# Kernel optimization log

Hardware: AMD Instinct MI355X
Metric: run time of the kernel (lower is better)

## Reference

```python
import jax, jax.numpy as jnp
import numpy as np

D_MODEL = 1024   # 'seq_len' arg = input feature dim
FF_DIM = 1024
SCALE = 0.03125  # 1/sqrt(1024)


def setup_inputs() -> dict:
    key = jax.random.key(0)
    ks = jax.random.split(key, 7)
    B, T = 8, 2048
    s = 1.0 / np.sqrt(D_MODEL)
    return {
        "sequence": jax.random.normal(ks[0], (B, T, D_MODEL), dtype=jnp.float32),
        "Wq": jax.random.uniform(ks[1], (FF_DIM, D_MODEL), jnp.float32, -s, s),
        "bq": jax.random.uniform(ks[2], (FF_DIM,), jnp.float32, -s, s),
        "Wk": jax.random.uniform(ks[3], (FF_DIM, D_MODEL), jnp.float32, -s, s),
        "bk": jax.random.uniform(ks[4], (FF_DIM,), jnp.float32, -s, s),
        "Wv": jax.random.uniform(ks[5], (FF_DIM, D_MODEL), jnp.float32, -s, s),
        "bv": jax.random.uniform(ks[6], (FF_DIM,), jnp.float32, -s, s),
    }


def reference(sequence, Wq, bq, Wk, bk, Wv, bv):
    # Q/K/V linear projections (torch Linear: x @ W.T + b)
    q = jnp.einsum('btd,fd->btf', sequence, Wq) + bq
    k = jnp.einsum('btd,fd->btf', sequence, Wk) + bk
    v = jnp.einsum('btd,fd->btf', sequence, Wv) + bv
    # scaled dot-product attention (dropout p=0 -> identity)
    scores = jnp.einsum('btf,bsf->bts', q, k) * SCALE  # [B,T,T]
    attn = jax.nn.softmax(scores, axis=-1)
    return jnp.einsum('bts,bsf->btf', attn, v)
```

## Files before the change

kernel.cpp:

```cpp
#include <hip/hip_runtime.h>
#include <hip/hip_bf16.h>

#define BB 8
#define TT 2048
#define DD 1024
#define FF 1024

typedef __attribute__((ext_vector_type(8))) short bf16x8;
typedef __attribute__((ext_vector_type(4))) float f32x4;
typedef __attribute__((ext_vector_type(4))) short s16x4;

constexpr float kScaleLog2e = 0.03125f * 1.44269504088896340736f;

__device__ __forceinline__ short bf16_bits(float x) {
    __hip_bfloat16 h = __float2bfloat16(x);
    short s;
    __builtin_memcpy(&s, &h, sizeof(short));
    return s;
}

__global__ __launch_bounds__(256) void cvt_kernel(
    const float* __restrict__ src, short* __restrict__ dst, int n8)
{
    const int i = blockIdx.x * 256 + threadIdx.x;
    if (i < n8) {
        f32x4 a = ((const f32x4*)src)[2 * i];
        f32x4 b = ((const f32x4*)src)[2 * i + 1];
        bf16x8 o;
#pragma unroll
        for (int j = 0; j < 4; ++j) { o[j] = bf16_bits(a[j]); o[4 + j] = bf16_bits(b[j]); }
        ((bf16x8*)dst)[i] = o;
    }
}

__device__ __forceinline__ void gemm_core(
    const short* __restrict__ A, int lda, int m0,
    const short* __restrict__ B, int ldb, int n0,
    int K, short* As, short* Bs, f32x4 acc[4][4])
{
    const int tid  = threadIdx.x;
    const int lane = tid & 63;
    const int w    = tid >> 6;
    const int wm   = (w & 1) * 64;
    const int wn   = (w >> 1) * 64;
    const int r    = lane & 15;
    const int qd   = lane >> 4;

    for (int k0 = 0; k0 < K; k0 += 32) {
        __syncthreads();
#pragma unroll
        for (int it = 0; it < 2; ++it) {
            const int s   = tid + it * 256;
            const int row = s >> 2;
            const int col = (s & 3) << 3;
            __builtin_amdgcn_global_load_lds(
                (const __attribute__((address_space(1))) unsigned int*)
                    (A + (size_t)(m0 + row) * lda + k0 + col),
                (__attribute__((address_space(3))) unsigned int*)(As + s * 8),
                16, 0, 0);
            __builtin_amdgcn_global_load_lds(
                (const __attribute__((address_space(1))) unsigned int*)
                    (B + (size_t)(n0 + row) * ldb + k0 + col),
                (__attribute__((address_space(3))) unsigned int*)(Bs + s * 8),
                16, 0, 0);
        }
        __syncthreads();
        bf16x8 af[4], bf[4];
#pragma unroll
        for (int m = 0; m < 4; ++m)
            af[m] = *(const bf16x8*)(As + (wm + m * 16 + r) * 32 + (qd << 3));
#pragma unroll
        for (int n = 0; n < 4; ++n)
            bf[n] = *(const bf16x8*)(Bs + (wn + n * 16 + r) * 32 + (qd << 3));
#pragma unroll
        for (int m = 0; m < 4; ++m)
#pragma unroll
            for (int n = 0; n < 4; ++n)
                acc[m][n] = __builtin_amdgcn_mfma_f32_16x16x32_bf16(af[m], bf[n], acc[m][n], 0, 0, 0);
    }
}

__global__ __launch_bounds__(256) void qkv_tiled(
    const short* __restrict__ seqb, const short* __restrict__ Wb,
    const float* __restrict__ bq, const float* __restrict__ bk,
    const float* __restrict__ bv,
    __hip_bfloat16* __restrict__ q, __hip_bfloat16* __restrict__ k,
    __hip_bfloat16* __restrict__ vT)
{
    __shared__ short As[128 * 32], Bs[128 * 32];
    const int bid  = blockIdx.x;
    const int mt   = bid / 24;
    const int rest = bid % 24;
    const int nt   = rest & 7;
    const int proj = rest >> 3;

    const short* W    = Wb + (size_t)proj * FF * DD;
    const float* bias = proj == 0 ? bq : (proj == 1 ? bk : bv);

    f32x4 acc[4][4];
#pragma unroll
    for (int m = 0; m < 4; ++m)
#pragma unroll
        for (int n = 0; n < 4; ++n) acc[m][n] = (f32x4){0.f, 0.f, 0.f, 0.f};

    gemm_core(seqb, DD, mt * 128, W, DD, nt * 128, DD, As, Bs, acc);

    const int lane = threadIdx.x & 63;
    const int w    = threadIdx.x >> 6;
    const int wm   = (w & 1) * 64;
    const int wn   = (w >> 1) * 64;
    const int r    = lane & 15;
    const int qd   = lane >> 4;
    const int row_base = mt * 128 + wm + qd * 4;
    const int col_base = nt * 128 + wn + r;

    if (proj < 2) {
        __hip_bfloat16* dst = (proj == 0) ? q : k;
#pragma unroll
        for (int n = 0; n < 4; ++n) {
            const int col = col_base + n * 16;
            const float bv_ = bias[col];
#pragma unroll
            for (int m = 0; m < 4; ++m)
#pragma unroll
                for (int i = 0; i < 4; ++i)
                    dst[(size_t)(row_base + m * 16 + i) * FF + col] =
                        __float2bfloat16(acc[m][n][i] + bv_);
        }
    } else {
#pragma unroll
        for (int m = 0; m < 4; ++m) {
            const int rowg = row_base + m * 16;
            const int b_   = rowg >> 11;
            const int t_   = rowg & 2047;
            __hip_bfloat16* vb = vT + (size_t)b_ * FF * TT;
#pragma unroll
            for (int n = 0; n < 4; ++n) {
                const int col = col_base + n * 16;
                const float bv_ = bias[col];
                s16x4 pack;
#pragma unroll
                for (int i = 0; i < 4; ++i) pack[i] = bf16_bits(acc[m][n][i] + bv_);
                *(s16x4*)(vb + (size_t)col * TT + t_) = pack;
            }
        }
    }
}

__global__ __launch_bounds__(256) void score_tiled(
    const __hip_bfloat16* __restrict__ q, const __hip_bfloat16* __restrict__ k,
    __hip_bfloat16* __restrict__ P, float* __restrict__ Z)
{
    __shared__ short As[128 * 32], Bs[128 * 32];
    const int bid = blockIdx.x;
    const int b   = bid >> 8;
    const int rem = bid & 255;
    const int tt  = rem >> 4;
    const int st  = rem & 15;

    const short* qb = (const short*)q + (size_t)b * TT * FF;
    const short* kb = (const short*)k + (size_t)b * TT * FF;

    f32x4 acc[4][4];
#pragma unroll
    for (int m = 0; m < 4; ++m)
#pragma unroll
        for (int n = 0; n < 4; ++n) acc[m][n] = (f32x4){0.f, 0.f, 0.f, 0.f};

    gemm_core(qb, FF, tt * 128, kb, FF, st * 128, FF, As, Bs, acc);

    const int lane = threadIdx.x & 63;
    const int w    = threadIdx.x >> 6;
    const int wm   = (w & 1) * 64;
    const int wn   = (w >> 1) * 64;
    const int r    = lane & 15;
    const int qd   = lane >> 4;
    const int row_base = tt * 128 + wm + qd * 4;
    const int col_base = st * 128 + wn + r;

    __hip_bfloat16* Pb = P + (size_t)b * TT * TT;
    float* Zb = Z + b * TT;

    float rs[4][4];
#pragma unroll
    for (int m = 0; m < 4; ++m)
#pragma unroll
        for (int i = 0; i < 4; ++i) rs[m][i] = 0.f;

#pragma unroll
    for (int m = 0; m < 4; ++m)
#pragma unroll
        for (int n = 0; n < 4; ++n) {
            const int col = col_base + n * 16;
#pragma unroll
            for (int i = 0; i < 4; ++i) {
                const float e = exp2f(acc[m][n][i] * kScaleLog2e);
                const __hip_bfloat16 eb = __float2bfloat16(e);
                rs[m][i] += __bfloat162float(eb);
                Pb[(size_t)(row_base + m * 16 + i) * TT + col] = eb;
            }
        }
#pragma unroll
    for (int off = 1; off < 16; off <<= 1)
#pragma unroll
        for (int m = 0; m < 4; ++m)
#pragma unroll
            for (int i = 0; i < 4; ++i) rs[m][i] += __shfl_xor(rs[m][i], off, 64);
    if (r == 0) {
#pragma unroll
        for (int m = 0; m < 4; ++m)
#pragma unroll
            for (int i = 0; i < 4; ++i)
                atomicAdd(&Zb[row_base + m * 16 + i], rs[m][i]);
    }
}

__global__ __launch_bounds__(256) void pv_tiled(
    const __hip_bfloat16* __restrict__ P, const __hip_bfloat16* __restrict__ vT,
    const float* __restrict__ Z, float* __restrict__ out)
{
    __shared__ short As[128 * 32], Bs[128 * 32];
    const int bid = blockIdx.x;
    const int b   = bid >> 7;
    const int rem = bid & 127;
    const int tt  = rem >> 3;
    const int ft  = rem & 7;

    const short* Pb = (const short*)P + (size_t)b * TT * TT;
    const short* vb = (const short*)vT + (size_t)b * FF * TT;

    f32x4 acc[4][4];
#pragma unroll
    for (int m = 0; m < 4; ++m)
#pragma unroll
        for (int n = 0; n < 4; ++n) acc[m][n] = (f32x4){0.f, 0.f, 0.f, 0.f};

    gemm_core(Pb, TT, tt * 128, vb, TT, ft * 128, TT, As, Bs, acc);

    const int lane = threadIdx.x & 63;
    const int w    = threadIdx.x >> 6;
    const int wm   = (w & 1) * 64;
    const int wn   = (w >> 1) * 64;
    const int r    = lane & 15;
    const int qd   = lane >> 4;
    const int row_base = tt * 128 + wm + qd * 4;
    const int col_base = ft * 128 + wn + r;

    const float* Zb = Z + b * TT;
    float* ob = out + (size_t)b * TT * FF;

#pragma unroll
    for (int m = 0; m < 4; ++m) {
        float rz[4];
#pragma unroll
        for (int i = 0; i < 4; ++i) rz[i] = 1.0f / Zb[row_base + m * 16 + i];
#pragma unroll
        for (int n = 0; n < 4; ++n) {
            const int col = col_base + n * 16;
#pragma unroll
            for (int i = 0; i < 4; ++i)
                ob[(size_t)(row_base + m * 16 + i) * FF + col] = acc[m][n][i] * rz[i];
        }
    }
}

extern "C" void kernel_launch(void* const* d_in, const int* in_sizes, int n_in,
                              void* d_out, int out_size, void* d_ws, size_t ws_size,
                              hipStream_t stream) {
    const float* seq = (const float*)d_in[0];
    const float* Wq  = (const float*)d_in[1];
    const float* bq  = (const float*)d_in[2];
    const float* Wk  = (const float*)d_in[3];
    const float* bk  = (const float*)d_in[4];
    const float* Wv  = (const float*)d_in[5];
    const float* bv  = (const float*)d_in[6];
    float* out = (float*)d_out;
    char* ws = (char*)d_ws;

    const size_t MB32 = 33554432;
    __hip_bfloat16* q   = (__hip_bfloat16*)(ws);
    __hip_bfloat16* k   = (__hip_bfloat16*)(ws + MB32);
    __hip_bfloat16* vT  = (__hip_bfloat16*)(ws + 2 * MB32);
    __hip_bfloat16* P   = (__hip_bfloat16*)(ws + 3 * MB32);
    float*          Z   = (float*)(ws + 3 * MB32 + (size_t)67108864);
    short*          seqb = (short*)P;
    short*          Wb   = (short*)((char*)P + MB32);

    hipMemsetAsync(Z, 0, (size_t)BB * TT * sizeof(float), stream);

    cvt_kernel<<<8192, 256, 0, stream>>>(seq, seqb, (BB * TT * DD) / 8);
    cvt_kernel<<<512, 256, 0, stream>>>(Wq, Wb,                         (FF * DD) / 8);
    cvt_kernel<<<512, 256, 0, stream>>>(Wk, Wb + (size_t)FF * DD,       (FF * DD) / 8);
    cvt_kernel<<<512, 256, 0, stream>>>(Wv, Wb + (size_t)2 * FF * DD,   (FF * DD) / 8);

    qkv_tiled<<<128 * 24, 256, 0, stream>>>(seqb, Wb, bq, bk, bv, q, k, vT);
    score_tiled<<<BB * 256, 256, 0, stream>>>(q, k, P, Z);
    pv_tiled<<<BB * 128, 256, 0, stream>>>(P, vT, Z, out);
}
```

Baseline: 469.2 us.

## Double K-tile depth to 64 with XOR-style LDS swizzle and merge conversion kernels

The GEMM core now stages 64-wide K slices per iteration instead of 32, which halves the number of barrier pairs per tile. LDS rows are stored with a rotation swizzle so the 16-byte fragment reads hit different banks and avoid conflicts. The four fp32-to-bf16 conversion launches are merged into a single launch. In exchange, LDS use per block doubles to 32KB, which may reduce occupancy.

```diff
diff --git a/kernel.cpp b/kernel.cpp
--- a/kernel.cpp
+++ b/kernel.cpp
@@ -19,18 +19,25 @@
     return s;
 }
 
-__global__ __launch_bounds__(256) void cvt_kernel(
-    const float* __restrict__ src, short* __restrict__ dst, int n8)
-{
-    const int i = blockIdx.x * 256 + threadIdx.x;
-    if (i < n8) {
-        f32x4 a = ((const f32x4*)src)[2 * i];
-        f32x4 b = ((const f32x4*)src)[2 * i + 1];
-        bf16x8 o;
-#pragma unroll
-        for (int j = 0; j < 4; ++j) { o[j] = bf16_bits(a[j]); o[4 + j] = bf16_bits(b[j]); }
-        ((bf16x8*)dst)[i] = o;
-    }
+__global__ __launch_bounds__(256) void cvt_all(
+    const float* __restrict__ seq, const float* __restrict__ Wq,
+    const float* __restrict__ Wk, const float* __restrict__ Wv,
+    short* __restrict__ seqb, short* __restrict__ Wb)
+{
+    const int bid = blockIdx.x;
+    const float* src;
+    short* dst;
+    int i;
+    if (bid < 8192)      { src = seq; dst = seqb;                      i = bid * 256 + threadIdx.x; }
+    else if (bid < 8704) { src = Wq;  dst = Wb;                        i = (bid - 8192) * 256 + threadIdx.x; }
+    else if (bid < 9216) { src = Wk;  dst = Wb + (size_t)FF * DD;      i = (bid - 8704) * 256 + threadIdx.x; }
+    else                 { src = Wv;  dst = Wb + (size_t)2 * FF * DD;  i = (bid - 9216) * 256 + threadIdx.x; }
+    f32x4 a = ((const f32x4*)src)[2 * i];
+    f32x4 b = ((const f32x4*)src)[2 * i + 1];
+    bf16x8 o;
+#pragma unroll
+    for (int j = 0; j < 4; ++j) { o[j] = bf16_bits(a[j]); o[4 + j] = bf16_bits(b[j]); }
+    ((bf16x8*)dst)[i] = o;
 }
 
 __device__ __forceinline__ void gemm_core(
@@ -46,13 +53,13 @@
     const int r    = lane & 15;
     const int qd   = lane >> 4;
 
-    for (int k0 = 0; k0 < K; k0 += 32) {
+    for (int k0 = 0; k0 < K; k0 += 64) {
         __syncthreads();
 #pragma unroll
-        for (int it = 0; it < 2; ++it) {
+        for (int it = 0; it < 4; ++it) {
             const int s   = tid + it * 256;
-            const int row = s >> 2;
-            const int col = (s & 3) << 3;
+            const int row = s >> 3;
+            const int col = (((s & 7) - (row & 7)) & 7) << 3;
             __builtin_amdgcn_global_load_lds(
                 (const __attribute__((address_space(1))) unsigned int*)
                     (A + (size_t)(m0 + row) * lda + k0 + col),
@@ -65,18 +72,25 @@
                 16, 0, 0);
         }
         __syncthreads();
-        bf16x8 af[4], bf[4];
-#pragma unroll
-        for (int m = 0; m < 4; ++m)
-            af[m] = *(const bf16x8*)(As + (wm + m * 16 + r) * 32 + (qd << 3));
-#pragma unroll
-        for (int n = 0; n < 4; ++n)
-            bf[n] = *(const bf16x8*)(Bs + (wn + n * 16 + r) * 32 + (qd << 3));
-#pragma unroll
-        for (int m = 0; m < 4; ++m)
-#pragma unroll
-            for (int n = 0; n < 4; ++n)
-                acc[m][n] = __builtin_amdgcn_mfma_f32_16x16x32_bf16(af[m], bf[n], acc[m][n], 0, 0, 0);
+#pragma unroll
+        for (int kk = 0; kk < 2; ++kk) {
+            bf16x8 af[4], bf[4];
+#pragma unroll
+            for (int m = 0; m < 4; ++m) {
+                const int R = wm + m * 16 + r;
+                af[m] = *(const bf16x8*)(As + R * 64 + (((kk * 4 + qd) + R) & 7) * 8);
+            }
+#pragma unroll
+            for (int n = 0; n < 4; ++n) {
+                const int R = wn + n * 16 + r;
+                bf[n] = *(const bf16x8*)(Bs + R * 64 + (((kk * 4 + qd) + R) & 7) * 8);
+            }
+#pragma unroll
+            for (int m = 0; m < 4; ++m)
+#pragma unroll
+                for (int n = 0; n < 4; ++n)
+                    acc[m][n] = __builtin_amdgcn_mfma_f32_16x16x32_bf16(af[m], bf[n], acc[m][n], 0, 0, 0);
+        }
     }
 }
 
@@ -87,7 +101,7 @@
     __hip_bfloat16* __restrict__ q, __hip_bfloat16* __restrict__ k,
     __hip_bfloat16* __restrict__ vT)
 {
-    __shared__ short As[128 * 32], Bs[128 * 32];
+    __shared__ short As[128 * 64], Bs[128 * 64];
     const int bid  = blockIdx.x;
     const int mt   = bid / 24;
     const int rest = bid % 24;
@@ -151,7 +165,7 @@
     const __hip_bfloat16* __restrict__ q, const __hip_bfloat16* __restrict__ k,
     __hip_bfloat16* __restrict__ P, float* __restrict__ Z)
 {
-    __shared__ short As[128 * 32], Bs[128 * 32];
+    __shared__ short As[128 * 64], Bs[128 * 64];
     const int bid = blockIdx.x;
     const int b   = bid >> 8;
     const int rem = bid & 255;
@@ -219,7 +233,7 @@
     const __hip_bfloat16* __restrict__ P, const __hip_bfloat16* __restrict__ vT,
     const float* __restrict__ Z, float* __restrict__ out)
 {
-    __shared__ short As[128 * 32], Bs[128 * 32];
+    __shared__ short As[128 * 64], Bs[128 * 64];
     const int bid = blockIdx.x;
     const int b   = bid >> 7;
     const int rem = bid & 127;
@@ -288,11 +302,7 @@
 
     hipMemsetAsync(Z, 0, (size_t)BB * TT * sizeof(float), stream);
 
-    cvt_kernel<<<8192, 256, 0, stream>>>(seq, seqb, (BB * TT * DD) / 8);
-    cvt_kernel<<<512, 256, 0, stream>>>(Wq, Wb,                         (FF * DD) / 8);
-    cvt_kernel<<<512, 256, 0, stream>>>(Wk, Wb + (size_t)FF * DD,       (FF * DD) / 8);
-    cvt_kernel<<<512, 256, 0, stream>>>(Wv, Wb + (size_t)2 * FF * DD,   (FF * DD) / 8);
-
+    cvt_all<<<9728, 256, 0, stream>>>(seq, Wq, Wk, Wv, seqb, Wb);
     qkv_tiled<<<128 * 24, 256, 0, stream>>>(seqb, Wb, bq, bk, bv, q, k, vT);
     score_tiled<<<BB * 256, 256, 0, stream>>>(q, k, P, Z);
     pv_tiled<<<BB * 128, 256, 0, stream>>>(P, vT, Z, out);
```

New measurement: 451.1 us. 3.8% less time.
